# Kernel tuning notes

Measured on AMD Instinct MI355X. Metric: run time of the kernel, lower is better.

## Reference

```python
import jax, jax.numpy as jnp
import numpy as np

B, T, N = 128, 1024, 64


def setup_inputs() -> dict:
    key = jax.random.key(0)
    k1, k2, k3, k4, k5 = jax.random.split(key, 5)
    potentials = jax.random.normal(k1, (B, T, N), dtype=jnp.float32)
    tags = jax.random.randint(k2, (B, T), 0, N, dtype=jnp.int32)
    # valid lengths in [T//2, T] so every sequence has at least one step
    sequence_length = jax.random.randint(k3, (B,), T // 2, T + 1, dtype=jnp.int32)
    chain_kernel = jax.random.normal(k4, (N, N), dtype=jnp.float32)
    sample_weight = jax.random.uniform(k5, (B,), dtype=jnp.float32)
    return {
        "potentials": potentials,
        "tags": tags,
        "sequence_length": sequence_length,
        "chain_kernel": chain_kernel,
        "sample_weight": sample_weight,
    }


def _crf_sequence_score(potentials, tags, sequence_length, chain_kernel):
    # potentials: [B,T,N], tags: [B,T] int, chain_kernel: [N,N]
    Bx, Tx, Nx = potentials.shape
    t_idx = jnp.arange(Tx)
    mask = (t_idx[None, :] < sequence_length[:, None]).astype(potentials.dtype)  # [B,T]
    # unary score: potentials at the gold tag per step
    unary = jnp.take_along_axis(potentials, tags[..., None].astype(jnp.int32), axis=2)[..., 0]  # [B,T]
    unary_score = jnp.sum(unary * mask, axis=1)  # [B]
    # binary score: transitions tag[t] -> tag[t+1], valid if t+1 < seq_len
    trans_sc = chain_kernel[tags[:, :-1], tags[:, 1:]]  # [B,T-1]
    binary_score = jnp.sum(trans_sc * mask[:, 1:], axis=1)  # [B]
    return unary_score + binary_score


def _crf_log_norm(potentials, sequence_length, chain_kernel):
    # forward algorithm with lax.scan over time
    Bx, Tx, Nx = potentials.shape
    alpha0 = potentials[:, 0]  # [B,N]
    pots_rest = jnp.transpose(potentials[:, 1:], (1, 0, 2))  # [T-1,B,N]
    step_mask = (jnp.arange(1, Tx)[:, None] < sequence_length[None, :])  # [T-1,B]

    def step(alpha, inp):
        pot_t, m_t = inp  # [B,N], [B]
        # logsumexp over previous tag: alpha[b,i] + trans[i,j]
        new = jax.nn.logsumexp(alpha[:, :, None] + chain_kernel[None], axis=1) + pot_t
        alpha = jnp.where(m_t[:, None], new, alpha)
        return alpha, None

    alpha_T, _ = jax.lax.scan(step, alpha0, (pots_rest, step_mask))
    return jax.nn.logsumexp(alpha_T, axis=1)  # [B]


def reference(potentials, tags, sequence_length, chain_kernel, sample_weight):
    seq_score = _crf_sequence_score(potentials, tags, sequence_length, chain_kernel)
    log_norm = _crf_log_norm(potentials, sequence_length, chain_kernel)
    log_likelihood = seq_score - log_norm  # [B]
    crf_loss = -log_likelihood * sample_weight
    return jnp.mean(crf_loss)
```

## Files before the change

kernel.cpp:

```cpp
#include <hip/hip_runtime.h>
#include <math.h>

#define BB 128
#define TT 1024
#define NN 64
#define NCH 16
#define SCH 64

typedef __attribute__((ext_vector_type(4))) float f32x4;
typedef __attribute__((ext_vector_type(4))) short bf16x4;

__device__ __forceinline__ float wave_sum64(float v) {
#pragma unroll
  for (int o = 32; o > 0; o >>= 1) v += __shfl_xor(v, o, 64);
  return v;
}

__device__ __forceinline__ unsigned pkbf(float lo, float hi) {
  unsigned a = __float_as_uint(lo) + 0x8000u;
  unsigned b = __float_as_uint(hi) + 0x8000u;
  return __builtin_amdgcn_perm(b, a, 0x07060302u);
}

__device__ __forceinline__ int fexp(float x) {
  unsigned u = __float_as_uint(x);
  int e = (int)((u >> 23) & 0xffu) - 127;
  if ((u & 0x7f800000u) == 0) e = 0;
  return e;
}

__global__ __launch_bounds__(64, 4) void crf_phase1(
    const float* __restrict__ pot, const int* __restrict__ tags,
    const int* __restrict__ seqlen, const float* __restrict__ K,
    unsigned* __restrict__ Hg, int* __restrict__ Eexp, float* __restrict__ score,
    float* __restrict__ accf, unsigned* __restrict__ cnt) {
  __shared__ __align__(16) float ring[4 * 64];
  __shared__ __align__(16) unsigned sht[544];
  const int lane = threadIdx.x;
  const int blk = blockIdx.x;

  if (blk == 0 && lane == 0) { *accf = 0.0f; *cnt = 0u; }

  if (blk < BB) {
    const int b = blk;
    const int L = seqlen[b];
    const int* tg = tags + b * TT;
    const float* pbase = pot + (size_t)b * TT * NN;
    float acc = 0.0f;
    for (int t = lane; t < TT; t += 64) {
      if (t < L) {
        int cc = tg[t];
        float u = pbase[(size_t)t * 64 + cc];
        float tr = (t >= 1) ? K[tg[t - 1] * 64 + cc] : 0.0f;
        acc += u + tr;
      }
    }
    acc = wave_sum64(acc);
    if (lane == 0) score[b] = acc;
    return;
  }

  const int idx = blk - BB;
  const int c = idx >> 9;
  const int b = (idx >> 2) & (BB - 1);
  const int g = idx & 3;
  const int L = seqlen[b];
  const int q = lane >> 4, lm = lane & 15;
  const int rb = q * 4;

  const int t0 = c * SCH + 1;
  const int tend = (L < TT) ? L : TT;
  int nsteps = tend - t0;
  if (nsteps > SCH) nsteps = SCH;

  unsigned* Hc = Hg + (size_t)(b * NCH + c) * 2048 + g * 8 * 64;
  if (nsteps <= 0) {
#pragma unroll
    for (int w = 0; w < 8; w++) {
      int c0 = g * 16 + 2 * w;
      unsigned v = (lane == c0 ? 0x3F80u : 0u) | (lane == c0 + 1 ? 0x3F800000u : 0u);
      Hc[w * 64 + lane] = v;
    }
    if (lane == 0) Eexp[(b * NCH + c) * 4 + g] = 0;
    return;
  }

  bf16x4 Af[4][4];
#pragma unroll
  for (int mt = 0; mt < 4; mt++)
#pragma unroll
    for (int kt = 0; kt < 4; kt++) {
      float v0 = __expf(K[(kt * 16 + rb + 0) * 64 + mt * 16 + lm]);
      float v1 = __expf(K[(kt * 16 + rb + 1) * 64 + mt * 16 + lm]);
      float v2 = __expf(K[(kt * 16 + rb + 2) * 64 + mt * 16 + lm]);
      float v3 = __expf(K[(kt * 16 + rb + 3) * 64 + mt * 16 + lm]);
      uint2 u; u.x = pkbf(v0, v1); u.y = pkbf(v2, v3);
      Af[mt][kt] = *(bf16x4*)&u;
    }

  f32x4 D[4];
#pragma unroll
  for (int mt = 0; mt < 4; mt++) {
    f32x4 d;
#pragma unroll
    for (int r = 0; r < 4; r++)
      d[r] = __expf(K[(g * 16 + lm) * 64 + mt * 16 + rb + r]);
    D[mt] = d;
  }

  const float* Pj = pot + (size_t)b * TT * NN + lane;
#pragma unroll
  for (int k = 0; k < 3; k++) {
    int tt = t0 + k; tt = tt > TT - 1 ? TT - 1 : tt;
    ring[k * 64 + lane] = __expf(Pj[(size_t)tt * NN]);
  }
  int t3 = t0 + 3 > TT - 1 ? TT - 1 : t0 + 3;
  int t4 = t0 + 4 > TT - 1 ? TT - 1 : t0 + 4;
  float rawq0 = Pj[(size_t)t3 * NN];
  float rawq1 = Pj[(size_t)t4 * NN];

  f32x4 pxc[4], pxn[4];
#pragma unroll
  for (int kt = 0; kt < 4; kt++)
    pxc[kt] = *(const f32x4*)&ring[0 * 64 + kt * 16 + rb];

  int etot = 0;
#pragma unroll 2
  for (int s = 0; s < nsteps - 1; s++) {
    if ((s & 7) == 7) {
      float d00 = __int_as_float(__builtin_amdgcn_readfirstlane(__float_as_int(D[0][0])));
      int e = fexp(d00);
      float psc = ldexpf(1.0f, -e);
      etot += e;
#pragma unroll
      for (int kt = 0; kt < 4; kt++) pxc[kt] *= psc;
    }
    bf16x4 Bf[4];
#pragma unroll
    for (int kt = 0; kt < 4; kt++) {
      f32x4 pr = D[kt] * pxc[kt];
      uint2 u;
      u.x = pkbf(pr[0], pr[1]);
      u.y = pkbf(pr[2], pr[3]);
      Bf[kt] = *(bf16x4*)&u;
    }
#pragma unroll
    for (int kt = 0; kt < 4; kt++)
      pxn[kt] = *(const f32x4*)&ring[((s + 1) & 3) * 64 + kt * 16 + rb];
    ring[((s + 3) & 3) * 64 + lane] = __expf(rawq0);
    rawq0 = rawq1;
    {
      int tn = t0 + s + 5; tn = tn > TT - 1 ? TT - 1 : tn;
      rawq1 = Pj[(size_t)tn * NN];
    }
#pragma unroll
    for (int mt = 0; mt < 4; mt++) {
      f32x4 acc = {0.f, 0.f, 0.f, 0.f};
#pragma unroll
      for (int kt = 0; kt < 4; kt++)
        acc = __builtin_amdgcn_mfma_f32_16x16x16bf16_1k(Af[mt][kt], Bf[kt], acc, 0, 0, 0);
      D[mt] = acc;
    }
#pragma unroll
    for (int kt = 0; kt < 4; kt++) pxc[kt] = pxn[kt];
  }

  {
    float hf = __int_as_float(
        __builtin_amdgcn_readfirstlane(__float_as_int(D[0][0] * pxc[0][0])));
    int ef = fexp(hf);
    float sc = ldexpf(1.0f, -ef);
    etot += ef;
#pragma unroll
    for (int mt = 0; mt < 4; mt++) {
      f32x4 d = D[mt]; f32x4 pv = pxc[mt];
      int base = lm * 33 + mt * 8 + q * 2;
      sht[base]     = pkbf(d[0] * pv[0] * sc, d[1] * pv[1] * sc);
      sht[base + 1] = pkbf(d[2] * pv[2] * sc, d[3] * pv[3] * sc);
    }
#pragma unroll
    for (int w = 0; w < 8; w++) {
      unsigned short a0 = ((const unsigned short*)(sht + (2 * w) * 33 + (lane >> 1)))[lane & 1];
      unsigned short a1 = ((const unsigned short*)(sht + (2 * w + 1) * 33 + (lane >> 1)))[lane & 1];
      Hc[w * 64 + lane] = (unsigned)a0 | ((unsigned)a1 << 16);
    }
    if (lane == 0) Eexp[(b * NCH + c) * 4 + g] = etot;
  }
}

__global__ __launch_bounds__(64, 4) void crf_phase2(
    const float* __restrict__ pot, const unsigned* __restrict__ Hg,
    const int* __restrict__ Eexp, const float* __restrict__ score,
    const float* __restrict__ wgt, float* __restrict__ accf,
    unsigned* __restrict__ cnt, float* __restrict__ out) {
  __shared__ __align__(16) float sha[64];
  const int j = threadIdx.x;
  const int b = blockIdx.x;

  float a = __expf(pot[(size_t)b * TT * NN + j]);
  sha[j] = a;
  int atot = 0;

  const unsigned* Hb = Hg + (size_t)b * NCH * 2048;
  unsigned bufA[32], bufB[32];
#pragma unroll
  for (int k = 0; k < 32; k++) bufA[k] = Hb[k * 64 + j];
#pragma unroll
  for (int k = 0; k < 32; k++) bufB[k] = Hb[2048 + k * 64 + j];

#pragma unroll
  for (int cc = 0; cc < NCH; cc += 2) {
#pragma unroll
    for (int half = 0; half < 2; half++) {
      const int c = cc + half;
      unsigned* cur = half ? bufB : bufA;
      float S[4] = {0.f, 0.f, 0.f, 0.f};
#pragma unroll
      for (int w4 = 0; w4 < 16; w4++) {
        f32x4 av = *(const f32x4*)&sha[w4 * 4];
        unsigned r0 = cur[2 * w4], r1 = cur[2 * w4 + 1];
        S[w4 >> 2] += __uint_as_float(r0 << 16) * av[0] +
                      __uint_as_float(r0 & 0xffff0000u) * av[1] +
                      __uint_as_float(r1 << 16) * av[2] +
                      __uint_as_float(r1 & 0xffff0000u) * av[3];
      }
      const int eb = b * 64 + c * 4;
      int e0 = Eexp[eb + 0], e1 = Eexp[eb + 1], e2 = Eexp[eb + 2], e3 = Eexp[eb + 3];
      int em = max(max(e0, e1), max(e2, e3));
      float Sc = ldexpf(S[0], e0 - em) + ldexpf(S[1], e1 - em) +
                 ldexpf(S[2], e2 - em) + ldexpf(S[3], e3 - em);
      int er = fexp(__int_as_float(
          __builtin_amdgcn_readfirstlane(__float_as_int(Sc))));
      a = ldexpf(Sc, -er);
      atot += em + er;
      sha[j] = a;
      if (c + 2 < NCH) {
        const unsigned* Hn = Hb + (size_t)(c + 2) * 2048;
#pragma unroll
        for (int k = 0; k < 32; k++) cur[k] = Hn[k * 64 + j];
      }
    }
  }

  float ssum = wave_sum64(a);
  if (j == 0) {
    float lognorm = __logf(ssum) + (float)atot * 0.69314718055994530942f;
    float loss = -(score[b] - lognorm) * wgt[b];
    atomicAdd(accf, loss * (1.0f / BB));
    __threadfence();
    unsigned old = atomicAdd(cnt, 1u);
    if (old == BB - 1) out[0] = atomicAdd(accf, 0.0f);
  }
}

__global__ __launch_bounds__(64) void crf_main_fb(
    const float* __restrict__ pot, const int* __restrict__ tags,
    const int* __restrict__ seqlen, const float* __restrict__ K,
    float* __restrict__ ws) {
  __shared__ float sh[4096];
  const int lane = threadIdx.x;
  const int blk = blockIdx.x;
  if (blk < BB) {
    const int b = blk;
    const int L = seqlen[b];
    float Ec[64];
#pragma unroll
    for (int i = 0; i < 64; i++) Ec[i] = __expf(K[i * 64 + lane]);
    const float* pb = pot + (size_t)b * TT * NN + lane;
    float av = __expf(pb[0]);
    int etot = 0;
    sh[lane] = av;
    float pf[8];
#pragma unroll
    for (int k = 0; k < 8; k++) pf[k] = pb[(size_t)(1 + k) * 64];
    for (int t0 = 1; t0 < L; t0 += 8) {
#pragma unroll
      for (int k = 0; k < 8; k++) {
        const int t = t0 + k;
        const float pe = __expf(pf[k]);
        int tn = t + 8; tn = tn > (TT - 1) ? (TT - 1) : tn;
        pf[k] = pb[(size_t)tn * 64];
        const float4* arow = (const float4*)(sh + ((t - 1) & 1) * 64);
        float s[8];
#pragma unroll
        for (int qq = 0; qq < 8; qq++) s[qq] = 0.0f;
#pragma unroll
        for (int qq = 0; qq < 16; qq++) {
          float4 a4 = arow[qq];
          float pr = fmaf(a4.x, Ec[4 * qq + 0], fmaf(a4.y, Ec[4 * qq + 1],
                     fmaf(a4.z, Ec[4 * qq + 2], a4.w * Ec[4 * qq + 3])));
          s[qq & 7] += pr;
        }
        float S = ((s[0] + s[1]) + (s[2] + s[3])) + ((s[4] + s[5]) + (s[6] + s[7]));
        if (t < L) {
          av = S * pe;
          if ((t & 3) == 0) {
            float m0 = __shfl(av, 0, 64);
            int e = ((__float_as_int(m0) >> 23) & 0xff) - 126;
            av = ldexpf(av, -e);
            etot += e;
          }
        }
        sh[(t & 1) * 64 + lane] = av;
      }
    }
    float ssum = wave_sum64(av);
    if (lane == 0) ws[b] = __logf(ssum) + (float)etot * 0.69314718055994530942f;
  } else {
    const int b = blk - BB;
    const int L = seqlen[b];
    for (int i = lane; i < 4096; i += 64) sh[i] = K[i];
    __syncthreads();
    const int* tg = tags + b * TT;
    const float* pbase = pot + (size_t)b * TT * NN;
    float acc = 0.0f;
    for (int t = lane; t < TT; t += 64) {
      if (t < L) {
        int cc = tg[t];
        float u = pbase[(size_t)t * 64 + cc];
        float tr = 0.0f;
        if (t >= 1) tr = sh[tg[t - 1] * 64 + cc];
        acc += u + tr;
      }
    }
    acc = wave_sum64(acc);
    if (lane == 0) ws[BB + b] = acc;
  }
}

__global__ __launch_bounds__(128) void crf_combine_fb(
    const float* __restrict__ ws, const float* __restrict__ wgt,
    float* __restrict__ out) {
  const int i = threadIdx.x;
  float lv = -(ws[BB + i] - ws[i]) * wgt[i];
  lv = wave_sum64(lv);
  __shared__ float p[2];
  if ((i & 63) == 0) p[i >> 6] = lv;
  __syncthreads();
  if (i == 0) out[0] = (p[0] + p[1]) * (1.0f / 128.0f);
}

extern "C" void kernel_launch(void* const* d_in, const int* in_sizes, int n_in,
                              void* d_out, int out_size, void* d_ws, size_t ws_size,
                              hipStream_t stream) {
  const float* pot    = (const float*)d_in[0];
  const int*   tags   = (const int*)d_in[1];
  const int*   seqlen = (const int*)d_in[2];
  const float* K      = (const float*)d_in[3];
  const float* wgt    = (const float*)d_in[4];

  const size_t HG_DW = (size_t)BB * NCH * 2048;
  const size_t NEXP  = (size_t)BB * NCH * 4;
  const size_t need  = (HG_DW + NEXP + BB + 2) * 4;

  if (ws_size >= need) {
    unsigned* Hg    = (unsigned*)d_ws;
    int* Eexp       = (int*)(Hg + HG_DW);
    float* score    = (float*)(Eexp + NEXP);
    float* accf     = score + BB;
    unsigned* cntp  = (unsigned*)(accf + 1);
    crf_phase1<<<BB + BB * NCH * 4, 64, 0, stream>>>(pot, tags, seqlen, K, Hg, Eexp,
                                                     score, accf, cntp);
    crf_phase2<<<BB, 64, 0, stream>>>(pot, Hg, Eexp, score, wgt, accf, cntp,
                                      (float*)d_out);
  } else {
    float* ws = (float*)d_ws;
    crf_main_fb<<<256, 64, 0, stream>>>(pot, tags, seqlen, K, ws);
    crf_combine_fb<<<1, 128, 0, stream>>>(ws, wgt, (float*)d_out);
  }
}
```

Baseline: 171.2 us.

## Pack four chunk waves per 256-thread block and reload ring operands in-loop

Phase 1 now launches 256-thread blocks, each holding four waves. In the chunk part, the four waves are the four column groups of one (batch, chunk) pair. In the score part, the four waves handle four batch rows. Each wave gets its own shared-memory slice, and the launch bounds move to 256 threads with 6 blocks per CU. The software-pipelined pxc/pxn register double-buffer is replaced by a direct shared-memory read of the current ring slot at the start of each step, with the loop unroll raised to 4. The aim is fewer, larger blocks and less block-scheduling and launch overhead, at the cost of register pressure under the new occupancy bound and the LDS read now sitting on the critical path.

Result: no change. 173.3 us (+1.2%).

```diff
diff --git a/kernel.cpp b/kernel.cpp
--- a/kernel.cpp
+++ b/kernel.cpp
@@ -29,20 +29,21 @@
   return e;
 }
 
-__global__ __launch_bounds__(64, 4) void crf_phase1(
+__global__ __launch_bounds__(256, 6) void crf_phase1(
     const float* __restrict__ pot, const int* __restrict__ tags,
     const int* __restrict__ seqlen, const float* __restrict__ K,
     unsigned* __restrict__ Hg, int* __restrict__ Eexp, float* __restrict__ score,
     float* __restrict__ accf, unsigned* __restrict__ cnt) {
-  __shared__ __align__(16) float ring[4 * 64];
-  __shared__ __align__(16) unsigned sht[544];
-  const int lane = threadIdx.x;
+  __shared__ __align__(16) unsigned char smem[4][2176];
+  const int tid = threadIdx.x;
+  const int wv = tid >> 6;
+  const int lane = tid & 63;
   const int blk = blockIdx.x;
 
-  if (blk == 0 && lane == 0) { *accf = 0.0f; *cnt = 0u; }
-
-  if (blk < BB) {
-    const int b = blk;
+  if (blk == 0 && tid == 0) { *accf = 0.0f; *cnt = 0u; }
+
+  if (blk < 32) {
+    const int b = blk * 4 + wv;
     const int L = seqlen[b];
     const int* tg = tags + b * TT;
     const float* pbase = pot + (size_t)b * TT * NN;
@@ -60,10 +61,10 @@
     return;
   }
 
-  const int idx = blk - BB;
-  const int c = idx >> 9;
-  const int b = (idx >> 2) & (BB - 1);
-  const int g = idx & 3;
+  const int idx = blk - 32;
+  const int c = idx >> 7;
+  const int b = idx & (BB - 1);
+  const int g = wv;
   const int L = seqlen[b];
   const int q = lane >> 4, lm = lane & 15;
   const int rb = q * 4;
@@ -108,6 +109,7 @@
     D[mt] = d;
   }
 
+  float* ring = (float*)smem[wv];
   const float* Pj = pot + (size_t)b * TT * NN + lane;
 #pragma unroll
   for (int k = 0; k < 3; k++) {
@@ -119,14 +121,14 @@
   float rawq0 = Pj[(size_t)t3 * NN];
   float rawq1 = Pj[(size_t)t4 * NN];
 
-  f32x4 pxc[4], pxn[4];
-#pragma unroll
-  for (int kt = 0; kt < 4; kt++)
-    pxc[kt] = *(const f32x4*)&ring[0 * 64 + kt * 16 + rb];
-
   int etot = 0;
-#pragma unroll 2
-  for (int s = 0; s < nsteps - 1; s++) {
+  const int nit = nsteps - 1;
+#pragma unroll 4
+  for (int s = 0; s < nit; s++) {
+    f32x4 pxc[4];
+#pragma unroll
+    for (int kt = 0; kt < 4; kt++)
+      pxc[kt] = *(const f32x4*)&ring[(s & 3) * 64 + kt * 16 + rb];
     if ((s & 7) == 7) {
       float d00 = __int_as_float(__builtin_amdgcn_readfirstlane(__float_as_int(D[0][0])));
       int e = fexp(d00);
@@ -144,9 +146,6 @@
       u.y = pkbf(pr[2], pr[3]);
       Bf[kt] = *(bf16x4*)&u;
     }
-#pragma unroll
-    for (int kt = 0; kt < 4; kt++)
-      pxn[kt] = *(const f32x4*)&ring[((s + 1) & 3) * 64 + kt * 16 + rb];
     ring[((s + 3) & 3) * 64 + lane] = __expf(rawq0);
     rawq0 = rawq1;
     {
@@ -161,19 +160,22 @@
         acc = __builtin_amdgcn_mfma_f32_16x16x16bf16_1k(Af[mt][kt], Bf[kt], acc, 0, 0, 0);
       D[mt] = acc;
     }
-#pragma unroll
-    for (int kt = 0; kt < 4; kt++) pxc[kt] = pxn[kt];
   }
 
   {
+    f32x4 pxl[4];
+#pragma unroll
+    for (int kt = 0; kt < 4; kt++)
+      pxl[kt] = *(const f32x4*)&ring[(nit & 3) * 64 + kt * 16 + rb];
     float hf = __int_as_float(
-        __builtin_amdgcn_readfirstlane(__float_as_int(D[0][0] * pxc[0][0])));
+        __builtin_amdgcn_readfirstlane(__float_as_int(D[0][0] * pxl[0][0])));
     int ef = fexp(hf);
     float sc = ldexpf(1.0f, -ef);
     etot += ef;
+    unsigned* sht = (unsigned*)smem[wv];
 #pragma unroll
     for (int mt = 0; mt < 4; mt++) {
-      f32x4 d = D[mt]; f32x4 pv = pxc[mt];
+      f32x4 d = D[mt]; f32x4 pv = pxl[mt];
       int base = lm * 33 + mt * 8 + q * 2;
       sht[base]     = pkbf(d[0] * pv[0] * sc, d[1] * pv[1] * sc);
       sht[base + 1] = pkbf(d[2] * pv[2] * sc, d[3] * pv[3] * sc);
@@ -359,8 +361,8 @@
     float* score    = (float*)(Eexp + NEXP);
     float* accf     = score + BB;
     unsigned* cntp  = (unsigned*)(accf + 1);
-    crf_phase1<<<BB + BB * NCH * 4, 64, 0, stream>>>(pot, tags, seqlen, K, Hg, Eexp,
-                                                     score, accf, cntp);
+    crf_phase1<<<32 + BB * NCH, 256, 0, stream>>>(pot, tags, seqlen, K, Hg, Eexp,
+                                                  score, accf, cntp);
     crf_phase2<<<BB, 64, 0, stream>>>(pot, Hg, Eexp, score, wgt, accf, cntp,
                                       (float*)d_out);
   } else {
```
